# Optimization experiments

Hardware: AMD Instinct MI355X
Metric: run time of the kernel (lower is better)

## Reference

```python
import jax, jax.numpy as jnp
import numpy as np

N = 8192       # tokens = batch x seq
D = 2048       # d_model
H = 2048       # per-expert hidden size
E = 8          # num_experts
TOP_K = 2


def setup_inputs() -> dict:
    key = jax.random.key(0)
    ks = jax.random.split(key, 6)
    x = jax.random.normal(ks[0], (N, D), dtype=jnp.float32)
    expert_weights = jax.random.uniform(ks[1], (N, TOP_K), dtype=jnp.float32)
    expert_indices = jax.random.randint(ks[2], (N, TOP_K), 0, E, dtype=jnp.int32)
    batch_size_per_expert = jnp.bincount(expert_indices.reshape(-1), length=E).astype(jnp.int32)
    scale = 0.02
    w1 = jax.random.normal(ks[3], (E, D, H), dtype=jnp.float32) * scale
    w2 = jax.random.normal(ks[4], (E, H, D), dtype=jnp.float32) * scale
    w3 = jax.random.normal(ks[5], (E, D, H), dtype=jnp.float32) * scale
    return {"x": x, "expert_weights": expert_weights, "expert_indices": expert_indices,
            "batch_size_per_expert": batch_size_per_expert, "w1": w1, "w2": w2, "w3": w3}


def reference(x, expert_weights, expert_indices, batch_size_per_expert, w1, w2, w3):
    """Math-equivalent to ParallelMLP.forward_once (non-EP path):
    sort tokens by expert, run per-expert SwiGLU MLP, unpermute and combine
    with top-k routing weights. Output does not depend on the sort order,
    so we express it as: out[t] = sum_k w[t,k] * expert_{idx[t,k]}(x[t]).
    """
    n, d = x.shape
    e = w1.shape[0]
    # Dense combine weights (n, E): scatter top-k routing weights.
    cw = jnp.zeros((n, e), x.dtype).at[jnp.arange(n)[:, None], expert_indices].add(expert_weights)
    out = jnp.zeros_like(x)
    for i in range(e):  # small fixed expert count
        h = jax.nn.silu(x @ w1[i]) * (x @ w3[i])  # (n, H) SwiGLU
        out = out + cw[:, i:i + 1] * (h @ w2[i])
    return out
```

## Files before the change

kernel.cpp:

```cpp
#include <hip/hip_runtime.h>
#include <stdint.h>

typedef unsigned short u16;
typedef __attribute__((ext_vector_type(8))) short s16x8;
typedef __attribute__((ext_vector_type(8))) unsigned short u16x8;
typedef __attribute__((ext_vector_type(4))) float f32x4;

#define N_TOK 8192
#define DDIM 2048
#define HDIM 2048
#define NROWS 16384
#define PADROWS 16640
#define MAXTILES 72
#define KTILES 32

#define W1T_OFF    0ull
#define W3T_OFF    67108864ull
#define W2T_OFF    134217728ull
#define XBF_OFF    201326592ull
#define HS_OFF     234881024ull
#define ROWTOK_OFF 303038464ull
#define POS_OFF    303107072ull
#define META_OFF   303172608ull
#define RES_OFF    0ull
#define WS_NEED    303172736ull

__device__ __forceinline__ u16 f2bf(float f) {
  union { float f; unsigned u; } v; v.f = f;
  unsigned r = v.u + 0x7fffu + ((v.u >> 16) & 1u);
  return (u16)(r >> 16);
}
__device__ __forceinline__ float bf2f(u16 u) {
  union { unsigned u; float f; } v; v.u = ((unsigned)u) << 16; return v.f;
}
__device__ __forceinline__ void gload_lds16(const u16* g, u16* l) {
  __builtin_amdgcn_global_load_lds(
      (const __attribute__((address_space(1))) unsigned int*)g,
      (__attribute__((address_space(3))) unsigned int*)l, 16, 0, 0);
}

__global__ void r1_kernel(const int* __restrict__ bsz, int* __restrict__ meta,
                          int* __restrict__ rowtok) {
  if (threadIdx.x == 0) {
    int off = 0, tbv = 0;
    meta[8] = 0; meta[17] = 0;
    for (int e = 0; e < 8; ++e) {
      meta[e] = 0;
      int c = bsz[e];
      off += c;  meta[9 + e] = off;
      tbv += (c + 255) >> 8; meta[18 + e] = tbv;
    }
  }
  for (int p = NROWS + (int)threadIdx.x; p < PADROWS; p += 256) rowtok[p] = 0;
}

__global__ void r2_kernel(const int* __restrict__ eidx, int* __restrict__ meta,
                          int* __restrict__ rowtok, int* __restrict__ posOf) {
  int i = blockIdx.x * 256 + threadIdx.x;
  int e = eidx[i];
  int p = atomicAdd(&meta[e], 1);
  int row = meta[8 + e] + p;
  rowtok[row] = i >> 1;
  posOf[i] = row;
}

__global__ void convert_x_kernel(const float* __restrict__ x, u16* __restrict__ xbf) {
  long long c = blockIdx.x * 256 + threadIdx.x;
  const float4 v0 = *(const float4*)&x[c * 8];
  const float4 v1 = *(const float4*)&x[c * 8 + 4];
  u16x8 u;
  u[0] = f2bf(v0.x); u[1] = f2bf(v0.y); u[2] = f2bf(v0.z); u[3] = f2bf(v0.w);
  u[4] = f2bf(v1.x); u[5] = f2bf(v1.y); u[6] = f2bf(v1.z); u[7] = f2bf(v1.w);
  *(u16x8*)&xbf[c * 8] = u;
}

__global__ __launch_bounds__(256) void transpose_cvt_kernel(
    const float* __restrict__ w1, const float* __restrict__ w2, const float* __restrict__ w3,
    u16* __restrict__ w1T, u16* __restrict__ w2T, u16* __restrict__ w3T) {
  __shared__ float tile[64][65];
  int z = blockIdx.z;
  const float* src; u16* dst;
  if (z < 8)        { src = w1 + (size_t)z * 4194304;        dst = w1T + (size_t)z * 4194304; }
  else if (z < 16)  { src = w3 + (size_t)(z - 8) * 4194304;  dst = w3T + (size_t)(z - 8) * 4194304; }
  else              { src = w2 + (size_t)(z - 16) * 4194304; dst = w2T + (size_t)(z - 16) * 4194304; }
  int r0 = blockIdx.y * 64, c0 = blockIdx.x * 64;
  int tid = threadIdx.x;
  int lr = tid >> 4, lc4 = (tid & 15) * 4;
#pragma unroll
  for (int i = 0; i < 4; ++i) {
    const float4 v = *(const float4*)&src[(size_t)(r0 + lr + i * 16) * 2048 + c0 + lc4];
    tile[lr + i * 16][lc4 + 0] = v.x; tile[lr + i * 16][lc4 + 1] = v.y;
    tile[lr + i * 16][lc4 + 2] = v.z; tile[lr + i * 16][lc4 + 3] = v.w;
  }
  __syncthreads();
  int orb = tid >> 3, oc8 = (tid & 7) * 8;
#pragma unroll
  for (int i = 0; i < 2; ++i) {
    int orow = orb + i * 32;
    u16x8 u;
#pragma unroll
    for (int j = 0; j < 8; ++j) u[j] = f2bf(tile[oc8 + j][orow]);
    *(u16x8*)&dst[(size_t)(c0 + orow) * 2048 + r0 + oc8] = u;
  }
}

template<int EPI>
__device__ __forceinline__ void gemm_body(
    const u16* __restrict__ A, const u16* __restrict__ B1m, const u16* __restrict__ B3m,
    const int* __restrict__ gather, const int* __restrict__ meta, u16* __restrict__ out) {
  const int* offs = meta + 8;
  const int* tb = meta + 17;

  const int nwg = (int)(gridDim.x * gridDim.y);
  const int lin = (int)(blockIdx.y * gridDim.x + blockIdx.x);
  const int q8 = nwg >> 3, r8 = nwg & 7;
  const int xcd = lin & 7, idx = lin >> 3;
  const int nl = (xcd < r8 ? xcd * (q8 + 1) : r8 * (q8 + 1) + (xcd - r8) * q8) + idx;
  const int tileId = nl % MAXTILES;
  const int colb = nl / MAXTILES;

  if (tileId >= tb[8]) return;
  int e = 0;
#pragma unroll
  for (int qq = 1; qq < 8; ++qq) if (tileId >= tb[qq]) e = qq;
  const int row0 = offs[e] + (tileId - tb[e]) * 256;
  const int vr = offs[e + 1] - row0;

  const int bRowA = EPI ? colb * 128 : colb * 256;
  const int bRowB = EPI ? colb * 128 : colb * 256 + 128;

  __shared__ u16 lds[2][4][8192];

  const int tid = threadIdx.x;
  const int wid = tid >> 6, lane = tid & 63;
  const int lm = lane & 15, kg = lane >> 4;
  const int wr = wid >> 2, wc = wid & 3;

  const u16* pA0[2]; const u16* pA1[2]; const u16* pB1[2]; const u16* pB3[2];
#pragma unroll
  for (int l = 0; l < 2; ++l) {
    int S = (wid * 2 + l) * 64 + lane;
    int r = S >> 3;
    int c8 = ((S & 7) ^ (r & 7)) * 8;
    int ga0 = row0 + r, ga1 = row0 + 128 + r;
    int ta0 = gather ? gather[ga0] : ga0;
    int ta1 = gather ? gather[ga1] : ga1;
    pA0[l] = A + (size_t)ta0 * 2048 + c8;
    pA1[l] = A + (size_t)ta1 * 2048 + c8;
    pB1[l] = B1m + ((size_t)e * 2048 + bRowA + r) * 2048 + c8;
    pB3[l] = B3m + ((size_t)e * 2048 + bRowB + r) * 2048 + c8;
  }

  int fA[2];
  fA[0] = lm * 64 + ((kg) ^ (lm & 7)) * 8;
  fA[1] = lm * 64 + ((4 + kg) ^ (lm & 7)) * 8;

  f32x4 acc1[8][2], acc3[8][2];
  f32x4 z4 = {0.f, 0.f, 0.f, 0.f};
#pragma unroll
  for (int m = 0; m < 8; ++m)
#pragma unroll
    for (int n = 0; n < 2; ++n) { acc1[m][n] = z4; acc3[m][n] = z4; }

#define STG(b, u, P) do { \
    gload_lds16(P[0], &lds[b][u][(wid * 2 + 0) * 512]); \
    gload_lds16(P[1], &lds[b][u][(wid * 2 + 1) * 512]); } while (0)
#define STG_ALL(b) do { STG(b, 0, pA0); STG(b, 1, pA1); \
    STG(b, 2, pB1); STG(b, 3, pB3); } while (0)
#define ADV() do { pA0[0]+=64; pA0[1]+=64; pA1[0]+=64; pA1[1]+=64; \
    pB1[0]+=64; pB1[1]+=64; pB3[0]+=64; pB3[1]+=64; } while (0)

  STG_ALL(0);
  ADV();

  s16x8 a[4][2], b1r[2][2], b3r[2][2];

#define READ_B() do { \
_Pragma("unroll") \
    for (int n = 0; n < 2; ++n) \
_Pragma("unroll") \
      for (int kk = 0; kk < 2; ++kk) { \
        b1r[n][kk] = *(const s16x8*)&lds[cur][2][wc * 2048 + n * 1024 + fA[kk]]; \
        b3r[n][kk] = *(const s16x8*)&lds[cur][3][wc * 2048 + n * 1024 + fA[kk]]; \
      } } while (0)
#define READ_A(half) do { \
_Pragma("unroll") \
    for (int mi = 0; mi < 4; ++mi) \
_Pragma("unroll") \
      for (int kk = 0; kk < 2; ++kk) \
        a[mi][kk] = *(const s16x8*)&lds[cur][wr][((half) * 4 + mi) * 1024 + fA[kk]]; \
    } while (0)
#define MFMA32(half) do { \
    __builtin_amdgcn_s_setprio(1); \
_Pragma("unroll") \
    for (int mi = 0; mi < 4; ++mi) \
_Pragma("unroll") \
      for (int n = 0; n < 2; ++n) { \
        acc1[(half)*4+mi][n] = __builtin_amdgcn_mfma_f32_16x16x32_bf16(a[mi][0], b1r[n][0], acc1[(half)*4+mi][n], 0, 0, 0); \
        acc1[(half)*4+mi][n] = __builtin_amdgcn_mfma_f32_16x16x32_bf16(a[mi][1], b1r[n][1], acc1[(half)*4+mi][n], 0, 0, 0); \
        acc3[(half)*4+mi][n] = __builtin_amdgcn_mfma_f32_16x16x32_bf16(a[mi][0], b3r[n][0], acc3[(half)*4+mi][n], 0, 0, 0); \
        acc3[(half)*4+mi][n] = __builtin_amdgcn_mfma_f32_16x16x32_bf16(a[mi][1], b3r[n][1], acc3[(half)*4+mi][n], 0, 0, 0); \
      } \
    __builtin_amdgcn_s_setprio(0); } while (0)

  for (int t = 0; t < KTILES - 1; ++t) {
    const int cur = t & 1;
    STG_ALL(cur ^ 1);
    ADV();
    asm volatile("s_waitcnt vmcnt(8)" ::: "memory");
    __builtin_amdgcn_s_barrier();
    READ_A(0);
    READ_B();
    MFMA32(0);
    __builtin_amdgcn_s_barrier();
    READ_A(1);
    MFMA32(1);
    __builtin_amdgcn_s_barrier();
  }
  {
    const int cur = (KTILES - 1) & 1;
    asm volatile("s_waitcnt vmcnt(0)" ::: "memory");
    __builtin_amdgcn_s_barrier();
    READ_A(0);
    READ_B();
    MFMA32(0);
    __builtin_amdgcn_s_barrier();
    READ_A(1);
    MFMA32(1);
  }

#pragma unroll
  for (int m = 0; m < 8; ++m)
#pragma unroll
    for (int n = 0; n < 2; ++n) {
      const int rloc = wr * 128 + m * 16 + kg * 4;
      if (EPI == 1) {
        const int col = colb * 128 + wc * 32 + n * 16 + lm;
#pragma unroll
        for (int rr = 0; rr < 4; ++rr) {
          int rowl = rloc + rr;
          if (rowl < vr) {
            float z = acc1[m][n][rr];
            float h = z / (1.f + __expf(-z)) * acc3[m][n][rr];
            out[(size_t)(row0 + rowl) * 2048 + col] = f2bf(h);
          }
        }
      } else {
        const int col = colb * 256 + wc * 32 + n * 16 + lm;
#pragma unroll
        for (int rr = 0; rr < 4; ++rr) {
          int rowl = rloc + rr;
          if (rowl < vr) {
            out[(size_t)(row0 + rowl) * 2048 + col] = f2bf(acc1[m][n][rr]);
            out[(size_t)(row0 + rowl) * 2048 + col + 128] = f2bf(acc3[m][n][rr]);
          }
        }
      }
    }
#undef STG
#undef STG_ALL
#undef ADV
#undef READ_B
#undef READ_A
#undef MFMA32
}

__global__ __launch_bounds__(512, 2) void gemm1_kernel(
    const u16* __restrict__ A, const u16* __restrict__ B1m, const u16* __restrict__ B3m,
    const int* __restrict__ gather, const int* __restrict__ meta, u16* __restrict__ out) {
  gemm_body<1>(A, B1m, B3m, gather, meta, out);
}
__global__ __launch_bounds__(512, 2) void gemm2_kernel(
    const u16* __restrict__ A, const u16* __restrict__ B1m, const u16* __restrict__ B3m,
    const int* __restrict__ gather, const int* __restrict__ meta, u16* __restrict__ out) {
  gemm_body<0>(A, B1m, B3m, gather, meta, out);
}

__global__ void combine_kernel(const u16* __restrict__ res, const int* __restrict__ posOf,
                               const float* __restrict__ ew, float* __restrict__ out) {
  int c = blockIdx.x * 256 + threadIdx.x;
  int t = c >> 8, dc = (c & 255) * 8;
  int p0 = posOf[2 * t], p1 = posOf[2 * t + 1];
  float wa = ew[2 * t], wb = ew[2 * t + 1];
  u16x8 u0 = *(const u16x8*)&res[(size_t)p0 * 2048 + dc];
  u16x8 u1 = *(const u16x8*)&res[(size_t)p1 * 2048 + dc];
  float4 o0, o1;
  o0.x = wa * bf2f(u0[0]) + wb * bf2f(u1[0]);
  o0.y = wa * bf2f(u0[1]) + wb * bf2f(u1[1]);
  o0.z = wa * bf2f(u0[2]) + wb * bf2f(u1[2]);
  o0.w = wa * bf2f(u0[3]) + wb * bf2f(u1[3]);
  o1.x = wa * bf2f(u0[4]) + wb * bf2f(u1[4]);
  o1.y = wa * bf2f(u0[5]) + wb * bf2f(u1[5]);
  o1.z = wa * bf2f(u0[6]) + wb * bf2f(u1[6]);
  o1.w = wa * bf2f(u0[7]) + wb * bf2f(u1[7]);
  *(float4*)&out[(size_t)t * 2048 + dc] = o0;
  *(float4*)&out[(size_t)t * 2048 + dc + 4] = o1;
}

extern "C" void kernel_launch(void* const* d_in, const int* in_sizes, int n_in,
                              void* d_out, int out_size, void* d_ws, size_t ws_size,
                              hipStream_t stream) {
  const float* x  = (const float*)d_in[0];
  const float* ew = (const float*)d_in[1];
  const int* eidx = (const int*)d_in[2];
  const int* bsz  = (const int*)d_in[3];
  const float* w1 = (const float*)d_in[4];
  const float* w2 = (const float*)d_in[5];
  const float* w3 = (const float*)d_in[6];
  float* out = (float*)d_out;
  char* ws = (char*)d_ws;

  if (ws_size < WS_NEED) {
    hipMemsetAsync(d_out, 0, (size_t)out_size * 4, stream);
    return;
  }

  u16* w1T = (u16*)(ws + W1T_OFF);
  u16* w3T = (u16*)(ws + W3T_OFF);
  u16* w2T = (u16*)(ws + W2T_OFF);
  u16* xbf = (u16*)(ws + XBF_OFF);
  u16* hs  = (u16*)(ws + HS_OFF);
  u16* res = (u16*)(ws + RES_OFF);
  int* rowtok = (int*)(ws + ROWTOK_OFF);
  int* posOf  = (int*)(ws + POS_OFF);
  int* meta   = (int*)(ws + META_OFF);

  r1_kernel<<<1, 256, 0, stream>>>(bsz, meta, rowtok);
  r2_kernel<<<64, 256, 0, stream>>>(eidx, meta, rowtok, posOf);
  convert_x_kernel<<<8192, 256, 0, stream>>>(x, xbf);
  transpose_cvt_kernel<<<dim3(32, 32, 24), 256, 0, stream>>>(w1, w2, w3, w1T, w2T, w3T);
  gemm1_kernel<<<dim3(MAXTILES, 16), 512, 0, stream>>>(xbf, w1T, w3T, rowtok, meta, hs);
  gemm2_kernel<<<dim3(MAXTILES, 8), 512, 0, stream>>>(hs, w2T, w2T, nullptr, meta, res);
  combine_kernel<<<8192, 256, 0, stream>>>(res, posOf, ew, out);
}
```

Measured before the change: 730.4 us.

## Split MFMA phases into finer LDS-read/compute stages with explicit lgkmcnt waits

Restructures the GEMM main loop into four smaller phases: B1 and B3 fragments are read separately and each feeds 16 MFMAs, with extra barriers and explicit lgkmcnt waits between phases. The last K-tile is folded into the loop under a conditional. The aim is to interleave LDS reads with MFMA work across the two waves per SIMD, ping-pong style, so register pressure and LDS latency are spread out. The cost is many more barriers per K-tile, which can stall the waves.

Measured after the change: 766.6 us. 1.05x slower.

```diff
diff --git a/kernel.cpp b/kernel.cpp
--- a/kernel.cpp
+++ b/kernel.cpp
@@ -175,14 +175,6 @@
 
   s16x8 a[4][2], b1r[2][2], b3r[2][2];
 
-#define READ_B() do { \
-_Pragma("unroll") \
-    for (int n = 0; n < 2; ++n) \
-_Pragma("unroll") \
-      for (int kk = 0; kk < 2; ++kk) { \
-        b1r[n][kk] = *(const s16x8*)&lds[cur][2][wc * 2048 + n * 1024 + fA[kk]]; \
-        b3r[n][kk] = *(const s16x8*)&lds[cur][3][wc * 2048 + n * 1024 + fA[kk]]; \
-      } } while (0)
 #define READ_A(half) do { \
 _Pragma("unroll") \
     for (int mi = 0; mi < 4; ++mi) \
@@ -190,43 +182,65 @@
       for (int kk = 0; kk < 2; ++kk) \
         a[mi][kk] = *(const s16x8*)&lds[cur][wr][((half) * 4 + mi) * 1024 + fA[kk]]; \
     } while (0)
-#define MFMA32(half) do { \
+#define READ_B1() do { \
+_Pragma("unroll") \
+    for (int n = 0; n < 2; ++n) \
+_Pragma("unroll") \
+      for (int kk = 0; kk < 2; ++kk) \
+        b1r[n][kk] = *(const s16x8*)&lds[cur][2][wc * 2048 + n * 1024 + fA[kk]]; \
+    } while (0)
+#define READ_B3() do { \
+_Pragma("unroll") \
+    for (int n = 0; n < 2; ++n) \
+_Pragma("unroll") \
+      for (int kk = 0; kk < 2; ++kk) \
+        b3r[n][kk] = *(const s16x8*)&lds[cur][3][wc * 2048 + n * 1024 + fA[kk]]; \
+    } while (0)
+#define MFMA16(ACC, half, B) do { \
     __builtin_amdgcn_s_setprio(1); \
 _Pragma("unroll") \
     for (int mi = 0; mi < 4; ++mi) \
 _Pragma("unroll") \
       for (int n = 0; n < 2; ++n) { \
-        acc1[(half)*4+mi][n] = __builtin_amdgcn_mfma_f32_16x16x32_bf16(a[mi][0], b1r[n][0], acc1[(half)*4+mi][n], 0, 0, 0); \
-        acc1[(half)*4+mi][n] = __builtin_amdgcn_mfma_f32_16x16x32_bf16(a[mi][1], b1r[n][1], acc1[(half)*4+mi][n], 0, 0, 0); \
-        acc3[(half)*4+mi][n] = __builtin_amdgcn_mfma_f32_16x16x32_bf16(a[mi][0], b3r[n][0], acc3[(half)*4+mi][n], 0, 0, 0); \
-        acc3[(half)*4+mi][n] = __builtin_amdgcn_mfma_f32_16x16x32_bf16(a[mi][1], b3r[n][1], acc3[(half)*4+mi][n], 0, 0, 0); \
+        ACC[(half)*4+mi][n] = __builtin_amdgcn_mfma_f32_16x16x32_bf16(a[mi][0], B[n][0], ACC[(half)*4+mi][n], 0, 0, 0); \
+        ACC[(half)*4+mi][n] = __builtin_amdgcn_mfma_f32_16x16x32_bf16(a[mi][1], B[n][1], ACC[(half)*4+mi][n], 0, 0, 0); \
       } \
     __builtin_amdgcn_s_setprio(0); } while (0)
-
-  for (int t = 0; t < KTILES - 1; ++t) {
+#define LGKM0() asm volatile("s_waitcnt lgkmcnt(0)" ::: "memory")
+
+  for (int t = 0; t < KTILES; ++t) {
     const int cur = t & 1;
-    STG_ALL(cur ^ 1);
-    ADV();
-    asm volatile("s_waitcnt vmcnt(8)" ::: "memory");
-    __builtin_amdgcn_s_barrier();
+    if (t + 1 < KTILES) {
+      STG_ALL(cur ^ 1);
+      ADV();
+      asm volatile("s_waitcnt vmcnt(8)" ::: "memory");
+    } else {
+      asm volatile("s_waitcnt vmcnt(0)" ::: "memory");
+    }
+    __builtin_amdgcn_s_barrier();
+
     READ_A(0);
-    READ_B();
-    MFMA32(0);
-    __builtin_amdgcn_s_barrier();
+    READ_B1();
+    asm volatile("s_waitcnt lgkmcnt(8)" ::: "memory");
+    __builtin_amdgcn_s_barrier();
+    LGKM0();
+    MFMA16(acc1, 0, b1r);
+    __builtin_amdgcn_s_barrier();
+
+    READ_B3();
+    __builtin_amdgcn_s_barrier();
+    LGKM0();
+    MFMA16(acc3, 0, b3r);
+    __builtin_amdgcn_s_barrier();
+
     READ_A(1);
-    MFMA32(1);
-    __builtin_amdgcn_s_barrier();
-  }
-  {
-    const int cur = (KTILES - 1) & 1;
-    asm volatile("s_waitcnt vmcnt(0)" ::: "memory");
-    __builtin_amdgcn_s_barrier();
-    READ_A(0);
-    READ_B();
-    MFMA32(0);
-    __builtin_amdgcn_s_barrier();
-    READ_A(1);
-    MFMA32(1);
+    __builtin_amdgcn_s_barrier();
+    LGKM0();
+    MFMA16(acc1, 1, b1r);
+    __builtin_amdgcn_s_barrier();
+
+    MFMA16(acc3, 1, b3r);
+    __builtin_amdgcn_s_barrier();
   }
 
 #pragma unroll
@@ -260,9 +274,11 @@
 #undef STG
 #undef STG_ALL
 #undef ADV
-#undef READ_B
 #undef READ_A
-#undef MFMA32
+#undef READ_B1
+#undef READ_B3
+#undef MFMA16
+#undef LGKM0
 }
 
 __global__ __launch_bounds__(512, 2) void gemm1_kernel(
```
